# Kernel tuning notes

Measured on AMD Instinct MI355X. Metric: run time of the kernel, lower is better.

The kernel has to match this reference:

```python
import jax, jax.numpy as jnp
import numpy as np

B, C, Hd, Wd = 8, 256, 64, 64
NUM_HEAD = 4
RATIO = 0.25
OUT_CH = int(NUM_HEAD * C * RATIO)      # 256
HEAD_DIM = OUT_CH // NUM_HEAD           # 64
EPS = 1e-5


def conv1x1(x, w, b=None):
    # x: [B,Ci,H,W], w: [Co,Ci]
    y = jnp.einsum('bchw,oc->bohw', x, w)
    if b is not None:
        y = y + b[None, :, None, None]
    return y


def setup_inputs() -> dict:
    key = jax.random.key(0)
    ks = jax.random.split(key, 16)
    s = lambda fan: 1.0 / np.sqrt(fan)
    return {
        'key':   jax.random.normal(ks[0], (B, C, Hd, Wd), jnp.float32),
        'query': jax.random.normal(ks[1], (B, C, Hd, Wd), jnp.float32),
        'wq': jax.random.normal(ks[2], (OUT_CH, C), jnp.float32) * s(C),
        'bq': jax.random.normal(ks[3], (OUT_CH,), jnp.float32) * 0.01,
        'wk': jax.random.normal(ks[4], (OUT_CH, C), jnp.float32) * s(C),
        'bk': jax.random.normal(ks[5], (OUT_CH,), jnp.float32) * 0.01,
        'wv': jax.random.normal(ks[6], (OUT_CH, C), jnp.float32) * s(C),
        'bv': jax.random.normal(ks[7], (OUT_CH,), jnp.float32) * 0.01,
        'wW': jax.random.normal(ks[8], (C, HEAD_DIM), jnp.float32) * s(HEAD_DIM),
        'bn_gamma': jnp.ones((C,), jnp.float32),
        'bn_beta': jnp.zeros((C,), jnp.float32),
        'bn_mean': jax.random.normal(ks[9], (C,), jnp.float32) * 0.1,
        'bn_var': jax.random.uniform(ks[10], (C,), jnp.float32, 0.5, 1.5),
        'w3': jax.random.normal(ks[11], (C, 2 * C, 3, 3), jnp.float32) * s(2 * C * 9),
        'b3': jax.random.normal(ks[12], (C,), jnp.float32) * 0.01,
        'w1': jax.random.normal(ks[13], (C, C), jnp.float32) * s(C),
        'b1': jax.random.normal(ks[14], (C,), jnp.float32) * 0.01,
    }


def reference(key, query, wq, bq, wk, bk, wv, bv, wW,
              bn_gamma, bn_beta, bn_mean, bn_var, w3, b3, w1, b1):
    b, c, h, w = query.shape
    q = conv1x1(query, wq, bq).reshape(b, NUM_HEAD, HEAD_DIM, h, w)
    k = conv1x1(key, wk, bk).reshape(b, NUM_HEAD, HEAD_DIM, h, w)
    v = conv1x1(key, wv, bv).reshape(b, NUM_HEAD, HEAD_DIM, h, w)

    att = (q * k).sum(axis=2) / np.sqrt(OUT_CH)          # [b, num_head, h, w]
    sm = jax.nn.softmax(att, axis=1)[:, :, None]         # softmax over heads
    weighted = (v * sm).sum(axis=1)                      # [b, head_dim, h, w]

    # W: 1x1 conv (no bias) + BatchNorm (inference)
    out = conv1x1(weighted, wW)
    inv = bn_gamma / jnp.sqrt(bn_var + EPS)
    out = out * inv[None, :, None, None] + (bn_beta - bn_mean * inv)[None, :, None, None]

    # fuse: ConvBlock (reflect-pad 3x3 conv + ELU) then 1x1 conv
    x = jnp.concatenate([key, out], axis=1)              # [b, 2C, h, w]
    x = jnp.pad(x, ((0, 0), (0, 0), (1, 1), (1, 1)), mode='reflect')
    x = jax.lax.conv_general_dilated(x, w3, (1, 1), 'VALID',
                                     dimension_numbers=('NCHW', 'OIHW', 'NCHW'))
    x = jax.nn.elu(x + b3[None, :, None, None])
    return conv1x1(x, w1, b1)
```

## Files before the change

### kernel.cpp

```cpp
#include <hip/hip_runtime.h>
#include <hip/hip_bf16.h>

typedef unsigned short u16;
typedef unsigned int u32;
typedef short bf16x8 __attribute__((ext_vector_type(8)));
typedef float f32x4 __attribute__((ext_vector_type(4)));

#define NPX 32768

__device__ __forceinline__ u16 f2bf(float f) {
  union { float f; u32 u; } v; v.f = f;
  return (u16)((v.u + 0x7FFFu + ((v.u >> 16) & 1u)) >> 16);
}

__device__ __forceinline__ void gload16(const u16* g, u16* l) {
  __builtin_amdgcn_global_load_lds(
      (const __attribute__((address_space(1))) void*)g,
      (__attribute__((address_space(3))) void*)l, 16, 0, 0);
}


__global__ __launch_bounds__(256) void prep_small(
    const float* __restrict__ wq, const float* __restrict__ wk,
    const float* __restrict__ wv, const float* __restrict__ w1,
    const float* __restrict__ wW, const float* __restrict__ gamma,
    const float* __restrict__ beta, const float* __restrict__ mean,
    const float* __restrict__ var,
    u16* __restrict__ wqb, u16* __restrict__ wkb, u16* __restrict__ wvb,
    u16* __restrict__ w1b, u16* __restrict__ wWpb, float* __restrict__ bWp) {
  int idx = blockIdx.x * 256 + threadIdx.x;
  if (idx < 65536) {
    int o = idx >> 8, c = idx & 255;
    int dst = (c >> 5) * 8192 + o * 32 + ((c >> 3) & 3) * 8 + (c & 7);
    wqb[dst] = f2bf(wq[idx]);
    wkb[dst] = f2bf(wk[idx]);
    wvb[dst] = f2bf(wv[idx]);
    w1b[dst] = f2bf(w1[idx]);
  } else if (idx < 65536 + 16384) {
    int j = idx - 65536;
    int o = j >> 6, c = j & 63;
    float inv = gamma[o] * rsqrtf(var[o] + 1e-5f);
    int dst = (c >> 5) * 8192 + o * 32 + ((c >> 3) & 3) * 8 + (c & 7);
    wWpb[dst] = f2bf(wW[j] * inv);
  } else if (idx < 65536 + 16384 + 256) {
    int o = idx - 65536 - 16384;
    float inv = gamma[o] * rsqrtf(var[o] + 1e-5f);
    bWp[o] = beta[o] - mean[o] * inv;
  }
}

__global__ __launch_bounds__(256) void prep_w3t(const float* __restrict__ w3,
                                                u16* __restrict__ w3c) {
  int idx = blockIdx.x * 256 + threadIdx.x;
  int o = idx >> 9, c = idx & 511;
  int cb = c >> 6, ks = (c >> 5) & 1, lk = (c >> 3) & 3, e = c & 7;
  #pragma unroll
  for (int t = 0; t < 9; ++t)
    w3c[(size_t)(((t * 8 + cb) * 2 + ks) * 256 + o) * 32 + lk * 8 + e] =
        f2bf(w3[idx * 9 + t]);
}

__global__ __launch_bounds__(256) void transpose_k(const float* __restrict__ src,
                                                   u16* __restrict__ dst,
                                                   int stride, int coff) {
  __shared__ u16 tile[64 * 72];
  int tid = threadIdx.x;
  int bid = blockIdx.x;
  int b = bid >> 8, rest = bid & 255;
  int c0 = (rest >> 6) * 64, px0 = (rest & 63) * 64;
  #pragma unroll
  for (int i = 0; i < 4; ++i) {
    int idx = tid + 256 * i;
    int c = idx >> 4, p4 = idx & 15;
    const float4 v = *(const float4*)&src[(size_t)(b * 256 + c0 + c) * 4096 + px0 + p4 * 4];
    u32 lo = f2bf(v.x) | ((u32)f2bf(v.y) << 16);
    u32 hi = f2bf(v.z) | ((u32)f2bf(v.w) << 16);
    *(uint2*)&tile[c * 72 + p4 * 4] = make_uint2(lo, hi);
  }
  __syncthreads();
  int px = tid >> 2, cq = tid & 3;
  u32 vv[8];
  #pragma unroll
  for (int i = 0; i < 8; ++i) {
    u16 a = tile[(cq * 16 + 2 * i) * 72 + px];
    u16 bb = tile[(cq * 16 + 2 * i + 1) * 72 + px];
    vv[i] = a | ((u32)bb << 16);
  }
  u16* dp = dst + (size_t)(b * 4096 + px0 + px) * stride + coff + c0 + cq * 16;
  *(uint4*)(dp) = make_uint4(vv[0], vv[1], vv[2], vv[3]);
  *(uint4*)(dp + 8) = make_uint4(vv[4], vv[5], vv[6], vv[7]);
}

__device__ __forceinline__ void gemm_k256(const u16* __restrict__ As,
                                          const u16* __restrict__ Bg,
                                          f32x4 acc[4][4], int lc, int lk, int wv_) {
  #pragma unroll
  for (int kk = 0; kk < 8; ++kk) {
    bf16x8 af[4], bfr[4];
    #pragma unroll
    for (int mi = 0; mi < 4; ++mi) {
      int px = mi * 16 + lc;
      int s = (kk * 4 + lk) ^ (px & 7);
      af[mi] = *(const bf16x8*)(As + px * 256 + s * 8);
    }
    #pragma unroll
    for (int nj = 0; nj < 4; ++nj) {
      int n = wv_ * 64 + nj * 16 + lc;
      bfr[nj] = *(const bf16x8*)(Bg + kk * 8192 + n * 32 + lk * 8);
    }
    #pragma unroll
    for (int mi = 0; mi < 4; ++mi)
      #pragma unroll
      for (int nj = 0; nj < 4; ++nj)
        acc[mi][nj] = __builtin_amdgcn_mfma_f32_16x16x32_bf16(af[mi], bfr[nj], acc[mi][nj], 0, 0, 0);
  }
}

__global__ __launch_bounds__(256, 2) void attn_kernel(
    const u16* __restrict__ xq, u16* __restrict__ xcat,
    const u16* __restrict__ wqb, const u16* __restrict__ wkb, const u16* __restrict__ wvb,
    const float* __restrict__ bq, const float* __restrict__ bk, const float* __restrict__ bv,
    const u16* __restrict__ wWpb, const float* __restrict__ bWp) {
  __shared__ __align__(16) char smem[74752];
  u16* aq = (u16*)smem;
  u16* ak = (u16*)(smem + 32768);
  float* att_s = (float*)(smem + 65536);
  u16* wsum = (u16*)(smem + 66560);
  float* wbuf = (float*)smem;

  int tid = threadIdx.x;
  int lane = tid & 63, wv_ = tid >> 6;
  int lc = lane & 15, lk = lane >> 4;
  int px0 = blockIdx.x * 64;

  #pragma unroll
  for (int i = 0; i < 8; ++i) {
    int idx = tid + 256 * i;
    int px = idx >> 5, c = idx & 31;
    int sc = c ^ (px & 7);
    *(uint4*)(aq + px * 256 + sc * 8) = *(const uint4*)(xq + (size_t)(px0 + px) * 256 + c * 8);
    *(uint4*)(ak + px * 256 + sc * 8) = *(const uint4*)(xcat + (size_t)(px0 + px) * 512 + c * 8);
  }
  __syncthreads();

  f32x4 zero4 = {0.f, 0.f, 0.f, 0.f};
  f32x4 accq[4][4], acck[4][4];
  #pragma unroll
  for (int mi = 0; mi < 4; ++mi)
    #pragma unroll
    for (int nj = 0; nj < 4; ++nj) { accq[mi][nj] = zero4; acck[mi][nj] = zero4; }

  gemm_k256(aq, wqb, accq, lc, lk, wv_);
  gemm_k256(ak, wkb, acck, lc, lk, wv_);

  #pragma unroll
  for (int nj = 0; nj < 4; ++nj) {
    float bqv = bq[wv_ * 64 + nj * 16 + lc];
    float bkv = bk[wv_ * 64 + nj * 16 + lc];
    #pragma unroll
    for (int mi = 0; mi < 4; ++mi)
      #pragma unroll
      for (int j = 0; j < 4; ++j) { accq[mi][nj][j] += bqv; acck[mi][nj][j] += bkv; }
  }

  float smx[4][4];
  #pragma unroll
  for (int mi = 0; mi < 4; ++mi)
    #pragma unroll
    for (int j = 0; j < 4; ++j) {
      float p = 0.f;
      #pragma unroll
      for (int nj = 0; nj < 4; ++nj) p += accq[mi][nj][j] * acck[mi][nj][j];
      p += __shfl_xor(p, 1);
      p += __shfl_xor(p, 2);
      p += __shfl_xor(p, 4);
      p += __shfl_xor(p, 8);
      float a = p * 0.0625f;
      smx[mi][j] = a;
      if (lc == 0) att_s[wv_ * 64 + mi * 16 + lk * 4 + j] = a;
    }
  __syncthreads();
  #pragma unroll
  for (int mi = 0; mi < 4; ++mi)
    #pragma unroll
    for (int j = 0; j < 4; ++j) {
      int px = mi * 16 + lk * 4 + j;
      float a0 = att_s[px], a1 = att_s[64 + px], a2 = att_s[128 + px], a3 = att_s[192 + px];
      float mx = fmaxf(fmaxf(a0, a1), fmaxf(a2, a3));
      float e0 = __expf(a0 - mx), e1 = __expf(a1 - mx);
      float e2 = __expf(a2 - mx), e3 = __expf(a3 - mx);
      float den = e0 + e1 + e2 + e3;
      float ew = wv_ == 0 ? e0 : (wv_ == 1 ? e1 : (wv_ == 2 ? e2 : e3));
      smx[mi][j] = ew / den;
    }

  f32x4 accv[4][4];
  #pragma unroll
  for (int mi = 0; mi < 4; ++mi)
    #pragma unroll
    for (int nj = 0; nj < 4; ++nj) accv[mi][nj] = zero4;
  gemm_k256(ak, wvb, accv, lc, lk, wv_);
  #pragma unroll
  for (int nj = 0; nj < 4; ++nj) {
    float bvv = bv[wv_ * 64 + nj * 16 + lc];
    #pragma unroll
    for (int mi = 0; mi < 4; ++mi)
      #pragma unroll
      for (int j = 0; j < 4; ++j) accv[mi][nj][j] += bvv;
  }
  __syncthreads();

  #pragma unroll
  for (int mi = 0; mi < 4; ++mi)
    #pragma unroll
    for (int nj = 0; nj < 4; ++nj)
      #pragma unroll
      for (int j = 0; j < 4; ++j) {
        int px = mi * 16 + lk * 4 + j;
        wbuf[(wv_ * 64 + px) * 64 + nj * 16 + lc] = smx[mi][j] * accv[mi][nj][j];
      }
  __syncthreads();

  #pragma unroll
  for (int i = 0; i < 2; ++i) {
    int idx = tid + 256 * i;
    int px = idx >> 3, c = idx & 7;
    float a8[8] = {0.f, 0.f, 0.f, 0.f, 0.f, 0.f, 0.f, 0.f};
    #pragma unroll
    for (int h = 0; h < 4; ++h) {
      const float4* p = (const float4*)(wbuf + ((h * 64 + px) * 64 + c * 8));
      float4 u0 = p[0], u1 = p[1];
      a8[0] += u0.x; a8[1] += u0.y; a8[2] += u0.z; a8[3] += u0.w;
      a8[4] += u1.x; a8[5] += u1.y; a8[6] += u1.z; a8[7] += u1.w;
    }
    u32 p0 = f2bf(a8[0]) | ((u32)f2bf(a8[1]) << 16);
    u32 p1 = f2bf(a8[2]) | ((u32)f2bf(a8[3]) << 16);
    u32 p2 = f2bf(a8[4]) | ((u32)f2bf(a8[5]) << 16);
    u32 p3 = f2bf(a8[6]) | ((u32)f2bf(a8[7]) << 16);
    *(uint4*)(wsum + px * 64 + (c ^ (px & 7)) * 8) = make_uint4(p0, p1, p2, p3);
  }
  __syncthreads();

  f32x4 a4[4][4];
  #pragma unroll
  for (int mi = 0; mi < 4; ++mi)
    #pragma unroll
    for (int nj = 0; nj < 4; ++nj) a4[mi][nj] = zero4;
  #pragma unroll
  for (int kk = 0; kk < 2; ++kk) {
    bf16x8 af[4], bfr[4];
    #pragma unroll
    for (int mi = 0; mi < 4; ++mi) {
      int px = mi * 16 + lc;
      int s = (kk * 4 + lk) ^ (px & 7);
      af[mi] = *(const bf16x8*)(wsum + px * 64 + s * 8);
    }
    #pragma unroll
    for (int nj = 0; nj < 4; ++nj) {
      int n = wv_ * 64 + nj * 16 + lc;
      bfr[nj] = *(const bf16x8*)(wWpb + kk * 8192 + n * 32 + lk * 8);
    }
    #pragma unroll
    for (int mi = 0; mi < 4; ++mi)
      #pragma unroll
      for (int nj = 0; nj < 4; ++nj)
        a4[mi][nj] = __builtin_amdgcn_mfma_f32_16x16x32_bf16(af[mi], bfr[nj], a4[mi][nj], 0, 0, 0);
  }
  #pragma unroll
  for (int nj = 0; nj < 4; ++nj) {
    int o = wv_ * 64 + nj * 16 + lc;
    float bb = bWp[o];
    #pragma unroll
    for (int mi = 0; mi < 4; ++mi)
      #pragma unroll
      for (int j = 0; j < 4; ++j) {
        int px = mi * 16 + lk * 4 + j;
        xcat[(size_t)(px0 + px) * 512 + 256 + o] = f2bf(a4[mi][nj][j] + bb);
      }
  }
}

__global__ __launch_bounds__(512, 2) void conv3_kernel(
    const u16* __restrict__ xcat, const u16* __restrict__ w3c,
    const float* __restrict__ b3, u16* __restrict__ elux) {
  extern __shared__ __align__(16) u16 smem[];
  u16* xb0 = smem;
  u16* xb1 = smem + 16896;
  u16* wb0 = smem + 33792;
  u16* wb1 = smem + 50176;

  int tid = threadIdx.x;
  int lane = tid & 63, wave = tid >> 6;
  int lc = lane & 15, lk = lane >> 4;
  int wr = wave >> 2, wc = wave & 3;
  int b = blockIdx.x >> 5, r0 = (blockIdx.x & 31) * 2;

  int gx[4], gxt;
  #pragma unroll
  for (int i = 0; i < 5; ++i) {
    int idx = (i < 4) ? (tid + i * 512) : (2048 + lane);
    int px = idx >> 3, t = idx & 7;
    int row = px / 66;
    int pxr = px - row * 66;
    int h_in = r0 - 1 + row; h_in = h_in < 0 ? 1 : (h_in > 63 ? 62 : h_in);
    int w_in = pxr - 1;      w_in = w_in < 0 ? 1 : (w_in > 63 ? 62 : w_in);
    int g = ((b * 64 + h_in) * 64 + w_in) * 512 + (t ^ (pxr & 7)) * 8;
    if (i < 4) gx[i] = g; else gxt = g;
  }
  int gw[4];
  #pragma unroll
  for (int i = 0; i < 4; ++i) {
    int p = tid + i * 512;
    int j = p ^ ((p >> 3) & 7);
    gw[i] = j * 8;
  }

#define STAGE_X(dst, cb_)                                                      \
  do {                                                                         \
    _Pragma("unroll") for (int i = 0; i < 4; ++i)                              \
        gload16(xcat + gx[i] + (cb_) * 64, (dst) + (size_t)(tid + i * 512) * 8); \
    if (wave == 0) gload16(xcat + gxt + (cb_) * 64, (dst) + (size_t)(2048 + lane) * 8); \
  } while (0)

#define STAGE_W(dst, slab)                                                     \
  do {                                                                         \
    const u16* wsrc = w3c + (size_t)(slab) * 16384;                            \
    _Pragma("unroll") for (int i = 0; i < 4; ++i)                              \
        gload16(wsrc + gw[i], (dst) + (size_t)(tid + i * 512) * 8);            \
  } while (0)

  f32x4 zero4 = {0.f, 0.f, 0.f, 0.f};
  f32x4 acc[4][4];
  #pragma unroll
  for (int mi = 0; mi < 4; ++mi)
    #pragma unroll
    for (int nj = 0; nj < 4; ++nj) acc[mi][nj] = zero4;

  STAGE_X(xb0, 0);
  STAGE_W(wb0, 0);
  __syncthreads();

  for (int cb = 0; cb < 8; ++cb) {
    const u16* xcur = (cb & 1) ? xb1 : xb0;
    #pragma unroll
    for (int tap = 0; tap < 9; ++tap) {
      const u16* wcur = ((cb + tap) & 1) ? wb1 : wb0;
      u16* wnxt = ((cb + tap) & 1) ? wb0 : wb1;
      if (tap < 8) {
        STAGE_W(wnxt, (tap + 1) * 8 + cb);
      } else if (cb < 7) {
        STAGE_W(wnxt, cb + 1);
        STAGE_X((cb & 1) ? xb0 : xb1, cb + 1);
      }
      const int dy = tap / 3, dx = tap % 3;
      #pragma unroll
      for (int ks = 0; ks < 2; ++ks) {
        bf16x8 af[4], bfr[4];
        #pragma unroll
        for (int mi = 0; mi < 4; ++mi) {
          int pp = mi * 16 + lc + dx;
          af[mi] = *(const bf16x8*)(xcur + ((wr + dy) * 66 + pp) * 64 +
                                    (((ks * 4 + lk) ^ (pp & 7)) * 8));
        }
        #pragma unroll
        for (int nj = 0; nj < 4; ++nj) {
          int n = wc * 64 + nj * 16 + lc;
          int j = ks * 1024 + n * 4 + lk;
          int p = j ^ ((j >> 3) & 7);
          bfr[nj] = *(const bf16x8*)(wcur + p * 8);
        }
        #pragma unroll
        for (int mi = 0; mi < 4; ++mi)
          #pragma unroll
          for (int nj = 0; nj < 4; ++nj)
            acc[mi][nj] = __builtin_amdgcn_mfma_f32_16x16x32_bf16(
                af[mi], bfr[nj], acc[mi][nj], 0, 0, 0);
      }
      __syncthreads();
    }
  }
#undef STAGE_X
#undef STAGE_W

  size_t rowbase = (size_t)((b * 64 + r0 + wr) * 64);
  #pragma unroll
  for (int nj = 0; nj < 4; ++nj) {
    int o = wc * 64 + nj * 16 + lc;
    float bias = b3[o];
    #pragma unroll
    for (int mi = 0; mi < 4; ++mi)
      #pragma unroll
      for (int j = 0; j < 4; ++j) {
        int w = mi * 16 + lk * 4 + j;
        float v = acc[mi][nj][j] + bias;
        v = v > 0.f ? v : (__expf(v) - 1.f);
        elux[(rowbase + w) * 256 + o] = f2bf(v);
      }
  }
}

__global__ __launch_bounds__(256, 3) void final_kernel(
    const u16* __restrict__ elux, const u16* __restrict__ w1b,
    const float* __restrict__ b1, float* __restrict__ out) {
  __shared__ __align__(16) u16 at[64 * 256];
  int tid = threadIdx.x;
  int lane = tid & 63, wv_ = tid >> 6;
  int lc = lane & 15, lk = lane >> 4;
  int px0 = blockIdx.x * 64;
  #pragma unroll
  for (int i = 0; i < 8; ++i) {
    int idx = tid + 256 * i;
    int px = idx >> 5, c = idx & 31;
    *(uint4*)(at + px * 256 + (c ^ (px & 7)) * 8) =
        *(const uint4*)(elux + (size_t)(px0 + px) * 256 + c * 8);
  }
  __syncthreads();
  f32x4 zero4 = {0.f, 0.f, 0.f, 0.f};
  f32x4 acc[4][4];
  #pragma unroll
  for (int mi = 0; mi < 4; ++mi)
    #pragma unroll
    for (int nj = 0; nj < 4; ++nj) acc[mi][nj] = zero4;
  gemm_k256(at, w1b, acc, lc, lk, wv_);
  int b = px0 >> 12;
  int hw0 = px0 & 4095;
  #pragma unroll
  for (int nj = 0; nj < 4; ++nj) {
    int o = wv_ * 64 + nj * 16 + lc;
    float bias = b1[o];
    #pragma unroll
    for (int mi = 0; mi < 4; ++mi) {
      float4 v;
      v.x = acc[mi][nj][0] + bias;
      v.y = acc[mi][nj][1] + bias;
      v.z = acc[mi][nj][2] + bias;
      v.w = acc[mi][nj][3] + bias;
      *(float4*)&out[(size_t)(b * 256 + o) * 4096 + hw0 + mi * 16 + lk * 4] = v;
    }
  }
}

extern "C" void kernel_launch(void* const* d_in, const int* in_sizes, int n_in,
                              void* d_out, int out_size, void* d_ws, size_t ws_size,
                              hipStream_t stream) {
  const float* key   = (const float*)d_in[0];
  const float* query = (const float*)d_in[1];
  const float* wq    = (const float*)d_in[2];
  const float* bq    = (const float*)d_in[3];
  const float* wk    = (const float*)d_in[4];
  const float* bk    = (const float*)d_in[5];
  const float* wv    = (const float*)d_in[6];
  const float* bv    = (const float*)d_in[7];
  const float* wW    = (const float*)d_in[8];
  const float* gamma = (const float*)d_in[9];
  const float* beta  = (const float*)d_in[10];
  const float* mean  = (const float*)d_in[11];
  const float* var   = (const float*)d_in[12];
  const float* w3    = (const float*)d_in[13];
  const float* b3    = (const float*)d_in[14];
  const float* w1    = (const float*)d_in[15];
  const float* b1    = (const float*)d_in[16];
  float* out = (float*)d_out;

  char* ws = (char*)d_ws;
  u16* x_q   = (u16*)(ws);
  u16* xcat  = (u16*)(ws + 16777216);
  u16* elux  = (u16*)(ws + 50331648);
  u16* w3t   = (u16*)(ws + 67108864);
  u16* wqb   = (u16*)(ws + 69468160);
  u16* wkb   = (u16*)(ws + 69599232);
  u16* wvb   = (u16*)(ws + 69730304);
  u16* w1b   = (u16*)(ws + 69861376);
  u16* wWpb  = (u16*)(ws + 69992448);
  float* bWp = (float*)(ws + 70025216);

  (void)hipFuncSetAttribute((const void*)conv3_kernel,
                            hipFuncAttributeMaxDynamicSharedMemorySize, 133120);

  prep_small<<<321, 256, 0, stream>>>(wq, wk, wv, w1, wW, gamma, beta, mean, var,
                                      wqb, wkb, wvb, w1b, wWpb, bWp);
  prep_w3t<<<512, 256, 0, stream>>>(w3, w3t);
  transpose_k<<<2048, 256, 0, stream>>>(query, x_q, 256, 0);
  transpose_k<<<2048, 256, 0, stream>>>(key, xcat, 512, 0);
  attn_kernel<<<512, 256, 0, stream>>>(x_q, xcat, wqb, wkb, wvb, bq, bk, bv, wWpb, bWp);
  conv3_kernel<<<256, 512, 133120, stream>>>(xcat, w3t, b3, elux);
  final_kernel<<<512, 256, 0, stream>>>(elux, w1b, b1, out);
}
```

Measured before the change: 136.2 us.

## Fuse input transposes into attention and final 1x1 conv into conv3 kernel

Removes the two standalone transpose kernels. The attention kernel now reads the fp32 query/key directly, converts them to bf16 and transposes them into LDS, and writes the key half of xcat itself. The final 1x1 conv is folded into the conv3 kernel, so the ELU output stays in LDS instead of making a round trip through global memory. The change also interleaves the Q and K GEMMs, stages the attention output through LDS for coalesced stores, and raises wave priority around the MFMA blocks. In exchange there are extra barriers in the attention load phase, more register pressure in the fused kernels, and fewer, longer kernels with less parallelism in the final GEMM.

After: 118.1 us. -13.3%, faster.

```diff
diff --git a/kernel.cpp b/kernel.cpp
--- a/kernel.cpp
+++ b/kernel.cpp
@@ -60,88 +60,60 @@
         f2bf(w3[idx * 9 + t]);
 }
 
-__global__ __launch_bounds__(256) void transpose_k(const float* __restrict__ src,
-                                                   u16* __restrict__ dst,
-                                                   int stride, int coff) {
-  __shared__ u16 tile[64 * 72];
-  int tid = threadIdx.x;
-  int bid = blockIdx.x;
-  int b = bid >> 8, rest = bid & 255;
-  int c0 = (rest >> 6) * 64, px0 = (rest & 63) * 64;
-  #pragma unroll
-  for (int i = 0; i < 4; ++i) {
-    int idx = tid + 256 * i;
-    int c = idx >> 4, p4 = idx & 15;
-    const float4 v = *(const float4*)&src[(size_t)(b * 256 + c0 + c) * 4096 + px0 + p4 * 4];
-    u32 lo = f2bf(v.x) | ((u32)f2bf(v.y) << 16);
-    u32 hi = f2bf(v.z) | ((u32)f2bf(v.w) << 16);
-    *(uint2*)&tile[c * 72 + p4 * 4] = make_uint2(lo, hi);
-  }
-  __syncthreads();
-  int px = tid >> 2, cq = tid & 3;
-  u32 vv[8];
-  #pragma unroll
-  for (int i = 0; i < 8; ++i) {
-    u16 a = tile[(cq * 16 + 2 * i) * 72 + px];
-    u16 bb = tile[(cq * 16 + 2 * i + 1) * 72 + px];
-    vv[i] = a | ((u32)bb << 16);
-  }
-  u16* dp = dst + (size_t)(b * 4096 + px0 + px) * stride + coff + c0 + cq * 16;
-  *(uint4*)(dp) = make_uint4(vv[0], vv[1], vv[2], vv[3]);
-  *(uint4*)(dp + 8) = make_uint4(vv[4], vv[5], vv[6], vv[7]);
-}
-
-__device__ __forceinline__ void gemm_k256(const u16* __restrict__ As,
-                                          const u16* __restrict__ Bg,
-                                          f32x4 acc[4][4], int lc, int lk, int wv_) {
-  #pragma unroll
-  for (int kk = 0; kk < 8; ++kk) {
-    bf16x8 af[4], bfr[4];
-    #pragma unroll
-    for (int mi = 0; mi < 4; ++mi) {
-      int px = mi * 16 + lc;
-      int s = (kk * 4 + lk) ^ (px & 7);
-      af[mi] = *(const bf16x8*)(As + px * 256 + s * 8);
-    }
-    #pragma unroll
-    for (int nj = 0; nj < 4; ++nj) {
-      int n = wv_ * 64 + nj * 16 + lc;
-      bfr[nj] = *(const bf16x8*)(Bg + kk * 8192 + n * 32 + lk * 8);
-    }
-    #pragma unroll
-    for (int mi = 0; mi < 4; ++mi)
-      #pragma unroll
-      for (int nj = 0; nj < 4; ++nj)
-        acc[mi][nj] = __builtin_amdgcn_mfma_f32_16x16x32_bf16(af[mi], bfr[nj], acc[mi][nj], 0, 0, 0);
-  }
-}
-
 __global__ __launch_bounds__(256, 2) void attn_kernel(
-    const u16* __restrict__ xq, u16* __restrict__ xcat,
+    const float* __restrict__ qsrc, const float* __restrict__ ksrc,
+    u16* __restrict__ xcat,
     const u16* __restrict__ wqb, const u16* __restrict__ wkb, const u16* __restrict__ wvb,
     const float* __restrict__ bq, const float* __restrict__ bk, const float* __restrict__ bv,
     const u16* __restrict__ wWpb, const float* __restrict__ bWp) {
   __shared__ __align__(16) char smem[74752];
   u16* aq = (u16*)smem;
   u16* ak = (u16*)(smem + 32768);
+  u16* tile = (u16*)(smem + 65536);
   float* att_s = (float*)(smem + 65536);
   u16* wsum = (u16*)(smem + 66560);
   float* wbuf = (float*)smem;
+  u16* ob = (u16*)smem;
 
   int tid = threadIdx.x;
   int lane = tid & 63, wv_ = tid >> 6;
   int lc = lane & 15, lk = lane >> 4;
   int px0 = blockIdx.x * 64;
-
-  #pragma unroll
-  for (int i = 0; i < 8; ++i) {
-    int idx = tid + 256 * i;
-    int px = idx >> 5, c = idx & 31;
-    int sc = c ^ (px & 7);
-    *(uint4*)(aq + px * 256 + sc * 8) = *(const uint4*)(xq + (size_t)(px0 + px) * 256 + c * 8);
-    *(uint4*)(ak + px * 256 + sc * 8) = *(const uint4*)(xcat + (size_t)(px0 + px) * 512 + c * 8);
-  }
-  __syncthreads();
+  int b = px0 >> 12, hw0 = px0 & 4095;
+
+  #pragma unroll
+  for (int t = 0; t < 8; ++t) {
+    const float* src = (t < 4) ? qsrc : ksrc;
+    int cc = t & 3;
+    #pragma unroll
+    for (int i = 0; i < 4; ++i) {
+      int idx = tid + 256 * i;
+      int c = idx >> 4, p4 = idx & 15;
+      const float4 v = *(const float4*)&src[(size_t)(b * 256 + cc * 64 + c) * 4096 + hw0 + p4 * 4];
+      u32 lo = f2bf(v.x) | ((u32)f2bf(v.y) << 16);
+      u32 hi = f2bf(v.z) | ((u32)f2bf(v.w) << 16);
+      *(uint2*)&tile[c * 72 + p4 * 4] = make_uint2(lo, hi);
+    }
+    __syncthreads();
+    int px = tid >> 2, cq = tid & 3;
+    u32 vv[8];
+    #pragma unroll
+    for (int i = 0; i < 8; ++i) {
+      u16 a = tile[(cq * 16 + 2 * i) * 72 + px];
+      u16 bb = tile[(cq * 16 + 2 * i + 1) * 72 + px];
+      vv[i] = a | ((u32)bb << 16);
+    }
+    u16* dstl = (t < 4) ? aq : ak;
+    int c8 = cc * 8 + cq * 2;
+    *(uint4*)(dstl + px * 256 + (c8 ^ (px & 7)) * 8) = make_uint4(vv[0], vv[1], vv[2], vv[3]);
+    *(uint4*)(dstl + px * 256 + ((c8 + 1) ^ (px & 7)) * 8) = make_uint4(vv[4], vv[5], vv[6], vv[7]);
+    if (t >= 4) {
+      u16* dp = xcat + (size_t)(px0 + px) * 512 + cc * 64 + cq * 16;
+      *(uint4*)dp = make_uint4(vv[0], vv[1], vv[2], vv[3]);
+      *(uint4*)(dp + 8) = make_uint4(vv[4], vv[5], vv[6], vv[7]);
+    }
+    __syncthreads();
+  }
 
   f32x4 zero4 = {0.f, 0.f, 0.f, 0.f};
   f32x4 accq[4][4], acck[4][4];
@@ -150,8 +122,30 @@
     #pragma unroll
     for (int nj = 0; nj < 4; ++nj) { accq[mi][nj] = zero4; acck[mi][nj] = zero4; }
 
-  gemm_k256(aq, wqb, accq, lc, lk, wv_);
-  gemm_k256(ak, wkb, acck, lc, lk, wv_);
+  #pragma unroll
+  for (int kk = 0; kk < 8; ++kk) {
+    bf16x8 afq[4], afk[4], bfq[4], bfk[4];
+    #pragma unroll
+    for (int mi = 0; mi < 4; ++mi) {
+      int px = mi * 16 + lc;
+      int s = (kk * 4 + lk) ^ (px & 7);
+      afq[mi] = *(const bf16x8*)(aq + px * 256 + s * 8);
+      afk[mi] = *(const bf16x8*)(ak + px * 256 + s * 8);
+    }
+    #pragma unroll
+    for (int nj = 0; nj < 4; ++nj) {
+      int n = wv_ * 64 + nj * 16 + lc;
+      bfq[nj] = *(const bf16x8*)(wqb + kk * 8192 + n * 32 + lk * 8);
+      bfk[nj] = *(const bf16x8*)(wkb + kk * 8192 + n * 32 + lk * 8);
+    }
+    #pragma unroll
+    for (int mi = 0; mi < 4; ++mi)
+      #pragma unroll
+      for (int nj = 0; nj < 4; ++nj) {
+        accq[mi][nj] = __builtin_amdgcn_mfma_f32_16x16x32_bf16(afq[mi], bfq[nj], accq[mi][nj], 0, 0, 0);
+        acck[mi][nj] = __builtin_amdgcn_mfma_f32_16x16x32_bf16(afk[mi], bfk[nj], acck[mi][nj], 0, 0, 0);
+      }
+  }
 
   #pragma unroll
   for (int nj = 0; nj < 4; ++nj) {
@@ -199,7 +193,26 @@
   for (int mi = 0; mi < 4; ++mi)
     #pragma unroll
     for (int nj = 0; nj < 4; ++nj) accv[mi][nj] = zero4;
-  gemm_k256(ak, wvb, accv, lc, lk, wv_);
+  #pragma unroll
+  for (int kk = 0; kk < 8; ++kk) {
+    bf16x8 af[4], bfr[4];
+    #pragma unroll
+    for (int mi = 0; mi < 4; ++mi) {
+      int px = mi * 16 + lc;
+      int s = (kk * 4 + lk) ^ (px & 7);
+      af[mi] = *(const bf16x8*)(ak + px * 256 + s * 8);
+    }
+    #pragma unroll
+    for (int nj = 0; nj < 4; ++nj) {
+      int n = wv_ * 64 + nj * 16 + lc;
+      bfr[nj] = *(const bf16x8*)(wvb + kk * 8192 + n * 32 + lk * 8);
+    }
+    #pragma unroll
+    for (int mi = 0; mi < 4; ++mi)
+      #pragma unroll
+      for (int nj = 0; nj < 4; ++nj)
+        accv[mi][nj] = __builtin_amdgcn_mfma_f32_16x16x32_bf16(af[mi], bfr[nj], accv[mi][nj], 0, 0, 0);
+  }
   #pragma unroll
   for (int nj = 0; nj < 4; ++nj) {
     float bvv = bv[wv_ * 64 + nj * 16 + lc];
@@ -275,14 +288,23 @@
       #pragma unroll
       for (int j = 0; j < 4; ++j) {
         int px = mi * 16 + lk * 4 + j;
-        xcat[(size_t)(px0 + px) * 512 + 256 + o] = f2bf(a4[mi][nj][j] + bb);
+        ob[px * 264 + o] = f2bf(a4[mi][nj][j] + bb);
       }
+  }
+  __syncthreads();
+  #pragma unroll
+  for (int i = 0; i < 8; ++i) {
+    int idx = tid + 256 * i;
+    int px = idx >> 5, c8 = idx & 31;
+    *(uint4*)(xcat + (size_t)(px0 + px) * 512 + 256 + c8 * 8) =
+        *(const uint4*)(ob + px * 264 + c8 * 8);
   }
 }
 
 __global__ __launch_bounds__(512, 2) void conv3_kernel(
     const u16* __restrict__ xcat, const u16* __restrict__ w3c,
-    const float* __restrict__ b3, u16* __restrict__ elux) {
+    const float* __restrict__ b3, const u16* __restrict__ w1b,
+    const float* __restrict__ b1, float* __restrict__ out) {
   extern __shared__ __align__(16) u16 smem[];
   u16* xb0 = smem;
   u16* xb1 = smem + 16896;
@@ -369,12 +391,14 @@
           int p = j ^ ((j >> 3) & 7);
           bfr[nj] = *(const bf16x8*)(wcur + p * 8);
         }
+        __builtin_amdgcn_s_setprio(1);
         #pragma unroll
         for (int mi = 0; mi < 4; ++mi)
           #pragma unroll
           for (int nj = 0; nj < 4; ++nj)
             acc[mi][nj] = __builtin_amdgcn_mfma_f32_16x16x32_bf16(
                 af[mi], bfr[nj], acc[mi][nj], 0, 0, 0);
+        __builtin_amdgcn_s_setprio(0);
       }
       __syncthreads();
     }
@@ -382,7 +406,7 @@
 #undef STAGE_X
 #undef STAGE_W
 
-  size_t rowbase = (size_t)((b * 64 + r0 + wr) * 64);
+  u16* eb = smem;
   #pragma unroll
   for (int nj = 0; nj < 4; ++nj) {
     int o = wc * 64 + nj * 16 + lc;
@@ -391,51 +415,46 @@
     for (int mi = 0; mi < 4; ++mi)
       #pragma unroll
       for (int j = 0; j < 4; ++j) {
-        int w = mi * 16 + lk * 4 + j;
+        int p = wr * 64 + mi * 16 + lk * 4 + j;
         float v = acc[mi][nj][j] + bias;
         v = v > 0.f ? v : (__expf(v) - 1.f);
-        elux[(rowbase + w) * 256 + o] = f2bf(v);
+        eb[p * 264 + o] = f2bf(v);
       }
   }
-}
-
-__global__ __launch_bounds__(256, 3) void final_kernel(
-    const u16* __restrict__ elux, const u16* __restrict__ w1b,
-    const float* __restrict__ b1, float* __restrict__ out) {
-  __shared__ __align__(16) u16 at[64 * 256];
-  int tid = threadIdx.x;
-  int lane = tid & 63, wv_ = tid >> 6;
-  int lc = lane & 15, lk = lane >> 4;
-  int px0 = blockIdx.x * 64;
-  #pragma unroll
-  for (int i = 0; i < 8; ++i) {
-    int idx = tid + 256 * i;
-    int px = idx >> 5, c = idx & 31;
-    *(uint4*)(at + px * 256 + (c ^ (px & 7)) * 8) =
-        *(const uint4*)(elux + (size_t)(px0 + px) * 256 + c * 8);
-  }
-  __syncthreads();
-  f32x4 zero4 = {0.f, 0.f, 0.f, 0.f};
-  f32x4 acc[4][4];
-  #pragma unroll
-  for (int mi = 0; mi < 4; ++mi)
-    #pragma unroll
-    for (int nj = 0; nj < 4; ++nj) acc[mi][nj] = zero4;
-  gemm_k256(at, w1b, acc, lc, lk, wv_);
-  int b = px0 >> 12;
-  int hw0 = px0 & 4095;
+  __syncthreads();
+
+  f32x4 acc2[4][4];
+  #pragma unroll
+  for (int mi = 0; mi < 4; ++mi)
+    #pragma unroll
+    for (int nj = 0; nj < 4; ++nj) acc2[mi][nj] = zero4;
+  #pragma unroll
+  for (int kk = 0; kk < 8; ++kk) {
+    bf16x8 af[4], bfr[4];
+    #pragma unroll
+    for (int mi = 0; mi < 4; ++mi)
+      af[mi] = *(const bf16x8*)(eb + (wr * 64 + mi * 16 + lc) * 264 + kk * 32 + lk * 8);
+    #pragma unroll
+    for (int nj = 0; nj < 4; ++nj)
+      bfr[nj] = *(const bf16x8*)(w1b + kk * 8192 + (wc * 64 + nj * 16 + lc) * 32 + lk * 8);
+    #pragma unroll
+    for (int mi = 0; mi < 4; ++mi)
+      #pragma unroll
+      for (int nj = 0; nj < 4; ++nj)
+        acc2[mi][nj] = __builtin_amdgcn_mfma_f32_16x16x32_bf16(af[mi], bfr[nj], acc2[mi][nj], 0, 0, 0);
+  }
   #pragma unroll
   for (int nj = 0; nj < 4; ++nj) {
-    int o = wv_ * 64 + nj * 16 + lc;
+    int o = wc * 64 + nj * 16 + lc;
     float bias = b1[o];
     #pragma unroll
     for (int mi = 0; mi < 4; ++mi) {
       float4 v;
-      v.x = acc[mi][nj][0] + bias;
-      v.y = acc[mi][nj][1] + bias;
-      v.z = acc[mi][nj][2] + bias;
-      v.w = acc[mi][nj][3] + bias;
-      *(float4*)&out[(size_t)(b * 256 + o) * 4096 + hw0 + mi * 16 + lk * 4] = v;
+      v.x = acc2[mi][nj][0] + bias;
+      v.y = acc2[mi][nj][1] + bias;
+      v.z = acc2[mi][nj][2] + bias;
+      v.w = acc2[mi][nj][3] + bias;
+      *(float4*)&out[(size_t)(b * 256 + o) * 4096 + (r0 + wr) * 64 + mi * 16 + lk * 4] = v;
     }
   }
 }
@@ -463,9 +482,7 @@
   float* out = (float*)d_out;
 
   char* ws = (char*)d_ws;
-  u16* x_q   = (u16*)(ws);
   u16* xcat  = (u16*)(ws + 16777216);
-  u16* elux  = (u16*)(ws + 50331648);
   u16* w3t   = (u16*)(ws + 67108864);
   u16* wqb   = (u16*)(ws + 69468160);
   u16* wkb   = (u16*)(ws + 69599232);
@@ -480,9 +497,7 @@
   prep_small<<<321, 256, 0, stream>>>(wq, wk, wv, w1, wW, gamma, beta, mean, var,
                                       wqb, wkb, wvb, w1b, wWpb, bWp);
   prep_w3t<<<512, 256, 0, stream>>>(w3, w3t);
-  transpose_k<<<2048, 256, 0, stream>>>(query, x_q, 256, 0);
-  transpose_k<<<2048, 256, 0, stream>>>(key, xcat, 512, 0);
-  attn_kernel<<<512, 256, 0, stream>>>(x_q, xcat, wqb, wkb, wvb, bq, bk, bv, wWpb, bWp);
-  conv3_kernel<<<256, 512, 133120, stream>>>(xcat, w3t, b3, elux);
-  final_kernel<<<512, 256, 0, stream>>>(elux, w1b, b1, out);
-}
+  attn_kernel<<<512, 256, 0, stream>>>(query, key, xcat, wqb, wkb, wvb,
+                                       bq, bk, bv, wWpb, bWp);
+  conv3_kernel<<<256, 512, 133120, stream>>>(xcat, w3t, b3, w1b, b1, out);
+}
```
